# Kernel optimization log

Hardware: AMD Instinct MI355X
Metric: run time of the kernel (lower is better)

Reference implementation:

```python
import jax, jax.numpy as jnp
import numpy as np

FT_SIZE = 512
NUM_BUCKETS = 8
HID = 32
IN_FEATS = 770

def _crelu(x):
    return jnp.clip(x, 0.0, 1.0)

def setup_inputs() -> dict:
    key = jax.random.key(0)
    ks = jax.random.split(key, 8)
    B = 65536
    x = jax.random.uniform(ks[0], (B, 2 * IN_FEATS), dtype=jnp.float32)
    s = 0.05
    ft_w = jax.random.normal(ks[1], (FT_SIZE, IN_FEATS), dtype=jnp.float32) * s
    ft_b = jax.random.normal(ks[2], (FT_SIZE,), dtype=jnp.float32) * s
    h1_w = jax.random.normal(ks[3], (NUM_BUCKETS, HID, 2 * FT_SIZE), dtype=jnp.float32) * s
    h1_b = jax.random.normal(ks[4], (NUM_BUCKETS, HID), dtype=jnp.float32) * s
    h2_w = jax.random.normal(ks[5], (NUM_BUCKETS, HID, HID), dtype=jnp.float32) * s
    h2_b = jax.random.normal(ks[6], (NUM_BUCKETS, HID), dtype=jnp.float32) * s
    h3_w = jax.random.normal(ks[7], (NUM_BUCKETS, 1, HID), dtype=jnp.float32) * s
    h3_b = jnp.zeros((NUM_BUCKETS, 1), dtype=jnp.float32)
    return {"x": x, "ft_w": ft_w, "ft_b": ft_b, "h1_w": h1_w, "h1_b": h1_b,
            "h2_w": h2_w, "h2_b": h2_b, "h3_w": h3_w, "h3_b": h3_b}

def reference(x, ft_w, ft_b, h1_w, h1_b, h2_w, h2_b, h3_w, h3_b):
    stm = x[:, :IN_FEATS]          # [B, 770]
    nstm = x[:, IN_FEATS:]         # [B, 770]
    stm_ft = _crelu(stm @ ft_w.T + ft_b)    # [B, FT]
    nstm_ft = _crelu(nstm @ ft_w.T + ft_b)  # [B, FT]
    combined = jnp.concatenate([stm_ft, nstm_ft], axis=1)  # [B, 2FT]
    # bucket index from piece count (STM first 768 channels)
    pc = jnp.sum(x[:, :768], axis=1)
    bucket_idx = jnp.clip((pc * NUM_BUCKETS / 33.0).astype(jnp.int32), 0, NUM_BUCKETS - 1)  # [B]
    # compute all bucket heads (dense compute-all, matching original loop+stack)
    h = _crelu(jnp.einsum('bi,koi->bko', combined, h1_w) + h1_b)  # [B, K, 32]
    h = _crelu(jnp.einsum('bko,kpo->bkp', h, h2_w) + h2_b)        # [B, K, 32]
    all_out = jnp.einsum('bko,kpo->bkp', h, h3_w) + h3_b          # [B, K, 1]
    out = jnp.take_along_axis(all_out, bucket_idx[:, None, None], axis=1)  # [B,1,1]
    return out[:, 0, :]  # [B, 1]
```

## Files before the change

### kernel.cpp

```cpp
#include <hip/hip_runtime.h>
#include <hip/hip_bf16.h>
#include <stdint.h>


#define INF  770
#define XROW 1540
#define KP   800
#define FT   512
#define K2   1024
#define N2   256

typedef _Float16 half8 __attribute__((ext_vector_type(8)));
typedef float floatx4 __attribute__((ext_vector_type(4)));
typedef float floatx2 __attribute__((ext_vector_type(2)));

__device__ __forceinline__ float crelu_f(float v) {
    return v < 0.f ? 0.f : (v > 1.f ? 1.f : v);
}

__device__ __forceinline__ void gl_lds16(const _Float16* g, _Float16* l) {
    __builtin_amdgcn_global_load_lds(
        (__attribute__((address_space(1))) void*)(uintptr_t)(const void*)g,
        (__attribute__((address_space(3))) void*)l,
        16, 0, 0);
}

__global__ __launch_bounds__(256) void convert_w_kernel(
    const float* __restrict__ ftw, const float* __restrict__ h1w,
    _Float16* __restrict__ ftw16, _Float16* __restrict__ h1w16)
{
    int idx = blockIdx.x * 256 + threadIdx.x;
    const int FTW = FT * KP;
    if (idx < FTW) {
        int r = idx / KP, c = idx - r * KP;
        ftw16[idx] = (_Float16)(c < INF ? ftw[r * INF + c] : 0.f);
    } else {
        int j = idx - FTW;
        if (j < N2 * K2) h1w16[j] = (_Float16)h1w[j];
    }
}

__global__ __launch_bounds__(512, 4) void gemm_ft_fused(
    const float* __restrict__ x,
    const _Float16* __restrict__ Bt,
    const float* __restrict__ bias,
    _Float16* __restrict__ C,
    int* __restrict__ bucket, int B)
{
    __shared__ _Float16 lsA[128 * 32];
    __shared__ _Float16 lsB[256 * 32];
    int bid = blockIdx.x;
    int xcd = bid & 7, g = bid >> 3;
    int nt = g & 1, mt = (g >> 1) * 8 + xcd;
    int m0 = mt * 128, n0 = nt * 256;
    int tid = threadIdx.x, lane = tid & 63, w = tid >> 6;
    int rm = (w & 1) * 64, rn = (w >> 1) * 64;
    int colL = lane & 15, rowQ = lane >> 4;
    int chA = rowQ ^ ((colL >> 1) & 3);

    int arow = tid >> 2, kq = tid & 3;
    const float* asrc = (m0 < B)
        ? x + (size_t)(m0 + arow) * XROW
        : x + (size_t)(m0 - B + arow) * XROW + INF;
    _Float16* adst = lsA + arow * 32 + (kq ^ ((arow >> 1) & 3)) * 8;

    floatx4 acc[4][4] = {};
    float psum = 0.f;

    for (int kt = 0; kt < 25; ++kt) {
        int ks = kt * 32;
        half8 hv = {};
        if (kt < 24) {
            const float* p = asrc + ks + kq * 8;
            floatx2 f0 = *(const floatx2*)(p);
            floatx2 f1 = *(const floatx2*)(p + 2);
            floatx2 f2 = *(const floatx2*)(p + 4);
            floatx2 f3 = *(const floatx2*)(p + 6);
            hv[0] = (_Float16)f0.x; hv[1] = (_Float16)f0.y;
            hv[2] = (_Float16)f1.x; hv[3] = (_Float16)f1.y;
            hv[4] = (_Float16)f2.x; hv[5] = (_Float16)f2.y;
            hv[6] = (_Float16)f3.x; hv[7] = (_Float16)f3.y;
            psum += (f0.x + f0.y) + (f1.x + f1.y) + (f2.x + f2.y) + (f3.x + f3.y);
        } else if (kq == 0) {
            floatx2 f0 = *(const floatx2*)(asrc + 768);
            hv[0] = (_Float16)f0.x; hv[1] = (_Float16)f0.y;
        }
        *(half8*)adst = hv;
        #pragma unroll
        for (int p = 0; p < 2; ++p) {
            int idx = p * 512 + tid;
            int br = idx >> 2, bs = (idx & 3) ^ ((br >> 1) & 3);
            gl_lds16(Bt + (size_t)(n0 + br) * KP + ks + bs * 8, lsB + idx * 8);
        }
        asm volatile("s_waitcnt vmcnt(0)" ::: "memory");
        __syncthreads();

        half8 af[4], bf[4];
        #pragma unroll
        for (int i = 0; i < 4; ++i)
            af[i] = *(const half8*)(lsA + (rm + i * 16 + colL) * 32 + chA * 8);
        #pragma unroll
        for (int j = 0; j < 4; ++j)
            bf[j] = *(const half8*)(lsB + (rn + j * 16 + colL) * 32 + chA * 8);
        #pragma unroll
        for (int i = 0; i < 4; ++i)
            #pragma unroll
            for (int j = 0; j < 4; ++j)
                acc[i][j] = __builtin_amdgcn_mfma_f32_16x16x32_f16(af[i], bf[j], acc[i][j], 0, 0, 0);
        __syncthreads();
    }

    psum += __shfl_xor(psum, 1, 64);
    psum += __shfl_xor(psum, 2, 64);
    if (nt == 0 && m0 < B && (tid & 3) == 0) {
        int bk = (int)(psum * (8.0f / 33.0f));
        bucket[m0 + arow] = bk < 0 ? 0 : (bk > 7 ? 7 : bk);
    }

    #pragma unroll
    for (int j = 0; j < 4; ++j) {
        int gn = n0 + rn + j * 16 + colL;
        float bv = bias[gn];
        #pragma unroll
        for (int i = 0; i < 4; ++i) {
            #pragma unroll
            for (int r = 0; r < 4; ++r) {
                int gm = m0 + rm + i * 16 + rowQ * 4 + r;
                C[(size_t)gm * FT + gn] = (_Float16)crelu_f(acc[i][j][r] + bv);
            }
        }
    }
}

__global__ __launch_bounds__(512, 4) void gemm_h1_kernel(
    const _Float16* __restrict__ C1,
    const _Float16* __restrict__ Bt,
    const float* __restrict__ bias,
    float* __restrict__ H,
    int B)
{
    __shared__ _Float16 lsA[64 * 32];
    __shared__ _Float16 lsB[256 * 32];
    int m0 = blockIdx.x * 64;
    int tid = threadIdx.x, lane = tid & 63, w = tid >> 6;
    int colL = lane & 15, rowQ = lane >> 4;
    int chA = rowQ ^ ((colL >> 1) & 3);

    floatx4 acc[4][2] = {};

    for (int kt = 0; kt < 32; ++kt) {
        int ks = kt * 32;
        const _Float16* Abase = (ks < FT) ? (C1 + (size_t)m0 * FT + ks)
                                          : (C1 + (size_t)(B + m0) * FT + (ks - FT));
        if (tid < 256) {
            int br = tid >> 2, bs = (tid & 3) ^ ((br >> 1) & 3);
            gl_lds16(Abase + (size_t)br * FT + bs * 8, lsA + tid * 8);
        }
        #pragma unroll
        for (int p = 0; p < 2; ++p) {
            int idx = p * 512 + tid;
            int br = idx >> 2, bs = (idx & 3) ^ ((br >> 1) & 3);
            gl_lds16(Bt + (size_t)br * K2 + ks + bs * 8, lsB + idx * 8);
        }
        asm volatile("s_waitcnt vmcnt(0)" ::: "memory");
        __syncthreads();

        half8 af[4], bf[2];
        #pragma unroll
        for (int i = 0; i < 4; ++i)
            af[i] = *(const half8*)(lsA + (i * 16 + colL) * 32 + chA * 8);
        #pragma unroll
        for (int j = 0; j < 2; ++j)
            bf[j] = *(const half8*)(lsB + (w * 32 + j * 16 + colL) * 32 + chA * 8);
        #pragma unroll
        for (int i = 0; i < 4; ++i)
            #pragma unroll
            for (int j = 0; j < 2; ++j)
                acc[i][j] = __builtin_amdgcn_mfma_f32_16x16x32_f16(af[i], bf[j], acc[i][j], 0, 0, 0);
        __syncthreads();
    }

    #pragma unroll
    for (int j = 0; j < 2; ++j) {
        int gn = w * 32 + j * 16 + colL;
        float bv = bias[gn];
        #pragma unroll
        for (int i = 0; i < 4; ++i) {
            #pragma unroll
            for (int r = 0; r < 4; ++r) {
                int gm = m0 + i * 16 + rowQ * 4 + r;
                H[(size_t)gm * N2 + gn] = crelu_f(acc[i][j][r] + bv);
            }
        }
    }
}

__global__ __launch_bounds__(256) void tail_kernel(
    const float* __restrict__ H,
    const int* __restrict__ bucket,
    const float* __restrict__ h2w,
    const float* __restrict__ h2b,
    const float* __restrict__ h3w,
    const float* __restrict__ h3b,
    float* __restrict__ out, int B)
{
    int s = blockIdx.x * 8 + (threadIdx.x >> 5);
    int j = threadIdx.x & 31;
    if (s >= B) return;
    int k = bucket[s];
    float h1v = H[(size_t)s * N2 + k * 32 + j];
    const float* w2 = h2w + ((k * 32 + j) * 32);
    float a = h2b[k * 32 + j];
    #pragma unroll
    for (int i = 0; i < 32; ++i) a += w2[i] * __shfl(h1v, i, 32);
    a = crelu_f(a);
    float p = a * h3w[k * 32 + j];
    #pragma unroll
    for (int off = 16; off; off >>= 1) p += __shfl_down(p, off, 32);
    if (j == 0) out[s] = p + h3b[k];
}

extern "C" void kernel_launch(void* const* d_in, const int* in_sizes, int n_in,
                              void* d_out, int out_size, void* d_ws, size_t ws_size,
                              hipStream_t stream) {
    const float* x    = (const float*)d_in[0];
    const float* ftw  = (const float*)d_in[1];
    const float* ftb  = (const float*)d_in[2];
    const float* h1w  = (const float*)d_in[3];
    const float* h1b  = (const float*)d_in[4];
    const float* h2w  = (const float*)d_in[5];
    const float* h2b  = (const float*)d_in[6];
    const float* h3w  = (const float*)d_in[7];
    const float* h3b  = (const float*)d_in[8];
    float* out = (float*)d_out;

    int B = in_sizes[0] / (2 * INF);

    char* ws = (char*)d_ws;
    _Float16* C1    = (_Float16*)ws;
    size_t c1_b     = (size_t)2 * B * FT * sizeof(_Float16);
    _Float16* ftw16 = (_Float16*)(ws + c1_b);
    size_t ftw_b    = (size_t)FT * KP * sizeof(_Float16);
    _Float16* h1w16 = (_Float16*)(ws + c1_b + ftw_b);
    size_t h1w_b    = (size_t)N2 * K2 * sizeof(_Float16);
    int* bucket     = (int*)(ws + c1_b + ftw_b + h1w_b);
    size_t bk_b     = (size_t)B * sizeof(int);
    float* H        = (float*)(ws + c1_b + ftw_b + h1w_b + bk_b);

    {
        int total = FT * KP + N2 * K2;
        convert_w_kernel<<<(total + 255) / 256, 256, 0, stream>>>(ftw, h1w, ftw16, h1w16);
    }
    gemm_ft_fused<<<(2 * B / 128) * 2, 512, 0, stream>>>(x, ftw16, ftb, C1, bucket, B);
    gemm_h1_kernel<<<B / 64, 512, 0, stream>>>(C1, h1w16, h1b, H, B);
    tail_kernel<<<(B + 7) / 8, 256, 0, stream>>>(H, bucket, h2w, h2b, h3w, h3b, out, B);
}
```

Measured before the change: 800.4 us.

## Double-buffer LDS tiles in both GEMMs and raise priority during MFMA

```diff
diff --git a/kernel.cpp b/kernel.cpp
--- a/kernel.cpp
+++ b/kernel.cpp
@@ -47,8 +47,8 @@
     _Float16* __restrict__ C,
     int* __restrict__ bucket, int B)
 {
-    __shared__ _Float16 lsA[128 * 32];
-    __shared__ _Float16 lsB[256 * 32];
+    __shared__ _Float16 lsA[2][128 * 32];
+    __shared__ _Float16 lsB[2][256 * 32];
     int bid = blockIdx.x;
     int xcd = bid & 7, g = bid >> 3;
     int nt = g & 1, mt = (g >> 1) * 8 + xcd;
@@ -62,52 +62,90 @@
     const float* asrc = (m0 < B)
         ? x + (size_t)(m0 + arow) * XROW
         : x + (size_t)(m0 - B + arow) * XROW + INF;
-    _Float16* adst = lsA + arow * 32 + (kq ^ ((arow >> 1) & 3)) * 8;
+    int aoff = arow * 32 + (kq ^ ((arow >> 1) & 3)) * 8;
 
     floatx4 acc[4][4] = {};
     float psum = 0.f;
-
-    for (int kt = 0; kt < 25; ++kt) {
-        int ks = kt * 32;
-        half8 hv = {};
-        if (kt < 24) {
-            const float* p = asrc + ks + kq * 8;
-            floatx2 f0 = *(const floatx2*)(p);
-            floatx2 f1 = *(const floatx2*)(p + 2);
-            floatx2 f2 = *(const floatx2*)(p + 4);
-            floatx2 f3 = *(const floatx2*)(p + 6);
-            hv[0] = (_Float16)f0.x; hv[1] = (_Float16)f0.y;
-            hv[2] = (_Float16)f1.x; hv[3] = (_Float16)f1.y;
-            hv[4] = (_Float16)f2.x; hv[5] = (_Float16)f2.y;
-            hv[6] = (_Float16)f3.x; hv[7] = (_Float16)f3.y;
-            psum += (f0.x + f0.y) + (f1.x + f1.y) + (f2.x + f2.y) + (f3.x + f3.y);
-        } else if (kq == 0) {
-            floatx2 f0 = *(const floatx2*)(asrc + 768);
-            hv[0] = (_Float16)f0.x; hv[1] = (_Float16)f0.y;
-        }
-        *(half8*)adst = hv;
-        #pragma unroll
-        for (int p = 0; p < 2; ++p) {
-            int idx = p * 512 + tid;
-            int br = idx >> 2, bs = (idx & 3) ^ ((br >> 1) & 3);
-            gl_lds16(Bt + (size_t)(n0 + br) * KP + ks + bs * 8, lsB + idx * 8);
-        }
-        asm volatile("s_waitcnt vmcnt(0)" ::: "memory");
-        __syncthreads();
-
+    floatx2 f0, f1, f2, f3, ae = {};
+
+    {
+        const float* pp = asrc + kq * 8;
+        f0 = *(const floatx2*)(pp);
+        f1 = *(const floatx2*)(pp + 2);
+        f2 = *(const floatx2*)(pp + 4);
+        f3 = *(const floatx2*)(pp + 6);
+    }
+    #pragma unroll
+    for (int q = 0; q < 2; ++q) {
+        int idx = q * 512 + tid;
+        int br = idx >> 2, bs = (idx & 3) ^ ((br >> 1) & 3);
+        gl_lds16(Bt + (size_t)(n0 + br) * KP + bs * 8, lsB[0] + idx * 8);
+    }
+    {
+        half8 hv;
+        hv[0] = (_Float16)f0.x; hv[1] = (_Float16)f0.y;
+        hv[2] = (_Float16)f1.x; hv[3] = (_Float16)f1.y;
+        hv[4] = (_Float16)f2.x; hv[5] = (_Float16)f2.y;
+        hv[6] = (_Float16)f3.x; hv[7] = (_Float16)f3.y;
+        psum += (f0.x + f0.y) + (f1.x + f1.y) + (f2.x + f2.y) + (f3.x + f3.y);
+        *(half8*)(lsA[0] + aoff) = hv;
+    }
+    {
+        const float* pp = asrc + 32 + kq * 8;
+        f0 = *(const floatx2*)(pp);
+        f1 = *(const floatx2*)(pp + 2);
+        f2 = *(const floatx2*)(pp + 4);
+        f3 = *(const floatx2*)(pp + 6);
+    }
+    __syncthreads();
+
+    int p = 0;
+    for (int t = 0; t < 25; ++t) {
+        if (t < 24) {
+            int ks = (t + 1) * 32;
+            #pragma unroll
+            for (int q = 0; q < 2; ++q) {
+                int idx = q * 512 + tid;
+                int br = idx >> 2, bs = (idx & 3) ^ ((br >> 1) & 3);
+                gl_lds16(Bt + (size_t)(n0 + br) * KP + ks + bs * 8,
+                         lsB[p ^ 1] + idx * 8);
+            }
+            half8 hv = {};
+            if (t < 23) {
+                hv[0] = (_Float16)f0.x; hv[1] = (_Float16)f0.y;
+                hv[2] = (_Float16)f1.x; hv[3] = (_Float16)f1.y;
+                hv[4] = (_Float16)f2.x; hv[5] = (_Float16)f2.y;
+                hv[6] = (_Float16)f3.x; hv[7] = (_Float16)f3.y;
+                psum += (f0.x + f0.y) + (f1.x + f1.y) + (f2.x + f2.y) + (f3.x + f3.y);
+            } else if (kq == 0) {
+                hv[0] = (_Float16)ae.x; hv[1] = (_Float16)ae.y;
+            }
+            *(half8*)(lsA[p ^ 1] + aoff) = hv;
+            if (t < 22) {
+                const float* pp = asrc + (t + 2) * 32 + kq * 8;
+                f0 = *(const floatx2*)(pp);
+                f1 = *(const floatx2*)(pp + 2);
+                f2 = *(const floatx2*)(pp + 4);
+                f3 = *(const floatx2*)(pp + 6);
+            } else if (t == 22) {
+                if (kq == 0) ae = *(const floatx2*)(asrc + 768);
+            }
+        }
         half8 af[4], bf[4];
         #pragma unroll
         for (int i = 0; i < 4; ++i)
-            af[i] = *(const half8*)(lsA + (rm + i * 16 + colL) * 32 + chA * 8);
+            af[i] = *(const half8*)(lsA[p] + (rm + i * 16 + colL) * 32 + chA * 8);
         #pragma unroll
         for (int j = 0; j < 4; ++j)
-            bf[j] = *(const half8*)(lsB + (rn + j * 16 + colL) * 32 + chA * 8);
+            bf[j] = *(const half8*)(lsB[p] + (rn + j * 16 + colL) * 32 + chA * 8);
+        __builtin_amdgcn_s_setprio(1);
         #pragma unroll
         for (int i = 0; i < 4; ++i)
             #pragma unroll
             for (int j = 0; j < 4; ++j)
                 acc[i][j] = __builtin_amdgcn_mfma_f32_16x16x32_f16(af[i], bf[j], acc[i][j], 0, 0, 0);
-        __syncthreads();
+        __builtin_amdgcn_s_setprio(0);
+        if (t < 24) { __syncthreads(); p ^= 1; }
     }
 
     psum += __shfl_xor(psum, 1, 64);
@@ -139,8 +177,8 @@
     float* __restrict__ H,
     int B)
 {
-    __shared__ _Float16 lsA[64 * 32];
-    __shared__ _Float16 lsB[256 * 32];
+    __shared__ _Float16 lsA[2][64 * 32];
+    __shared__ _Float16 lsB[2][256 * 32];
     int m0 = blockIdx.x * 64;
     int tid = threadIdx.x, lane = tid & 63, w = tid >> 6;
     int colL = lane & 15, rowQ = lane >> 4;
@@ -148,36 +186,43 @@
 
     floatx4 acc[4][2] = {};
 
-    for (int kt = 0; kt < 32; ++kt) {
+    auto stage = [&](int kt, int b) {
         int ks = kt * 32;
         const _Float16* Abase = (ks < FT) ? (C1 + (size_t)m0 * FT + ks)
                                           : (C1 + (size_t)(B + m0) * FT + (ks - FT));
         if (tid < 256) {
             int br = tid >> 2, bs = (tid & 3) ^ ((br >> 1) & 3);
-            gl_lds16(Abase + (size_t)br * FT + bs * 8, lsA + tid * 8);
-        }
-        #pragma unroll
-        for (int p = 0; p < 2; ++p) {
-            int idx = p * 512 + tid;
+            gl_lds16(Abase + (size_t)br * FT + bs * 8, lsA[b] + tid * 8);
+        }
+        #pragma unroll
+        for (int q = 0; q < 2; ++q) {
+            int idx = q * 512 + tid;
             int br = idx >> 2, bs = (idx & 3) ^ ((br >> 1) & 3);
-            gl_lds16(Bt + (size_t)br * K2 + ks + bs * 8, lsB + idx * 8);
-        }
-        asm volatile("s_waitcnt vmcnt(0)" ::: "memory");
-        __syncthreads();
-
+            gl_lds16(Bt + (size_t)br * K2 + ks + bs * 8, lsB[b] + idx * 8);
+        }
+    };
+
+    stage(0, 0);
+    __syncthreads();
+
+    int p = 0;
+    for (int t = 0; t < 32; ++t) {
+        if (t < 31) stage(t + 1, p ^ 1);
         half8 af[4], bf[2];
         #pragma unroll
         for (int i = 0; i < 4; ++i)
-            af[i] = *(const half8*)(lsA + (i * 16 + colL) * 32 + chA * 8);
+            af[i] = *(const half8*)(lsA[p] + (i * 16 + colL) * 32 + chA * 8);
         #pragma unroll
         for (int j = 0; j < 2; ++j)
-            bf[j] = *(const half8*)(lsB + (w * 32 + j * 16 + colL) * 32 + chA * 8);
+            bf[j] = *(const half8*)(lsB[p] + (w * 32 + j * 16 + colL) * 32 + chA * 8);
+        __builtin_amdgcn_s_setprio(1);
         #pragma unroll
         for (int i = 0; i < 4; ++i)
             #pragma unroll
             for (int j = 0; j < 2; ++j)
                 acc[i][j] = __builtin_amdgcn_mfma_f32_16x16x32_f16(af[i], bf[j], acc[i][j], 0, 0, 0);
-        __syncthreads();
+        __builtin_amdgcn_s_setprio(0);
+        if (t < 31) { __syncthreads(); p ^= 1; }
     }
 
     #pragma unroll
```

Result: slower. 1.204 ms (+50.4%).

## Pre-convert x to fp16 and triple-buffer LDS in both GEMMs

Applied to the files above, without the earlier changes.

```diff
diff --git a/kernel.cpp b/kernel.cpp
--- a/kernel.cpp
+++ b/kernel.cpp
@@ -1,5 +1,4 @@
 #include <hip/hip_runtime.h>
-#include <hip/hip_bf16.h>
 #include <stdint.h>
 
 
@@ -11,8 +10,9 @@
 #define N2   256
 
 typedef _Float16 half8 __attribute__((ext_vector_type(8)));
+typedef _Float16 half4 __attribute__((ext_vector_type(4)));
+typedef _Float16 half2v __attribute__((ext_vector_type(2)));
 typedef float floatx4 __attribute__((ext_vector_type(4)));
-typedef float floatx2 __attribute__((ext_vector_type(2)));
 
 __device__ __forceinline__ float crelu_f(float v) {
     return v < 0.f ? 0.f : (v > 1.f ? 1.f : v);
@@ -24,6 +24,11 @@
         (__attribute__((address_space(3))) void*)l,
         16, 0, 0);
 }
+
+#define VMCNT(n) asm volatile("s_waitcnt vmcnt(" #n ")" ::: "memory")
+#define BAR() do { asm volatile("" ::: "memory"); \
+                   __builtin_amdgcn_s_barrier(); \
+                   asm volatile("" ::: "memory"); } while (0)
 
 __global__ __launch_bounds__(256) void convert_w_kernel(
     const float* __restrict__ ftw, const float* __restrict__ h1w,
@@ -40,15 +45,53 @@
     }
 }
 
-__global__ __launch_bounds__(512, 4) void gemm_ft_fused(
-    const float* __restrict__ x,
-    const _Float16* __restrict__ Bt,
+__global__ __launch_bounds__(256) void convert_x_kernel(
+    const float* __restrict__ x, _Float16* __restrict__ x16,
+    int* __restrict__ bucket, int B)
+{
+    int r = blockIdx.x * 4 + (threadIdx.x >> 6);
+    int l = threadIdx.x & 63;
+    const float* xr = x + (size_t)r * XROW;
+    _Float16* stm = x16 + (size_t)r * KP;
+    _Float16* nst = x16 + (size_t)(B + r) * KP;
+    float psum = 0.f;
+    for (int j = l; j < 385; j += 64) {
+        floatx4 f = *(const floatx4*)(xr + j * 4);
+        int c = j * 4;
+        if (j < 192) psum += (f.x + f.y) + (f.z + f.w);
+        if (c + 3 < INF) {
+            half4 hv = {(_Float16)f.x, (_Float16)f.y, (_Float16)f.z, (_Float16)f.w};
+            *(half4*)(stm + c) = hv;
+        } else if (c < INF) {
+            stm[768] = (_Float16)f.x; stm[769] = (_Float16)f.y;
+            nst[0]   = (_Float16)f.z; nst[1]  = (_Float16)f.w;
+        } else {
+            int cc = c - INF;
+            half2v h0 = {(_Float16)f.x, (_Float16)f.y};
+            half2v h1 = {(_Float16)f.z, (_Float16)f.w};
+            *(half2v*)(nst + cc) = h0;
+            *(half2v*)(nst + cc + 2) = h1;
+        }
+    }
+    half2v z = {};
+    if (l < 15)                *(half2v*)(stm + INF + 2 * l) = z;
+    else if (l >= 16 && l < 31) *(half2v*)(nst + INF + 2 * (l - 16)) = z;
+    #pragma unroll
+    for (int off = 1; off < 64; off <<= 1) psum += __shfl_xor(psum, off, 64);
+    if (l == 0) {
+        int bk = (int)(psum * (8.0f / 33.0f));
+        bucket[r] = bk < 0 ? 0 : (bk > 7 ? 7 : bk);
+    }
+}
+
+__global__ __launch_bounds__(512, 4) void gemm_ft_p(
+    const _Float16* __restrict__ A,
+    const _Float16* __restrict__ Bw,
     const float* __restrict__ bias,
-    _Float16* __restrict__ C,
-    int* __restrict__ bucket, int B)
-{
-    __shared__ _Float16 lsA[128 * 32];
-    __shared__ _Float16 lsB[256 * 32];
+    _Float16* __restrict__ C)
+{
+    __shared__ _Float16 lsA[3][128 * 32];
+    __shared__ _Float16 lsB[3][256 * 32];
     int bid = blockIdx.x;
     int xcd = bid & 7, g = bid >> 3;
     int nt = g & 1, mt = (g >> 1) * 8 + xcd;
@@ -58,64 +101,58 @@
     int colL = lane & 15, rowQ = lane >> 4;
     int chA = rowQ ^ ((colL >> 1) & 3);
 
-    int arow = tid >> 2, kq = tid & 3;
-    const float* asrc = (m0 < B)
-        ? x + (size_t)(m0 + arow) * XROW
-        : x + (size_t)(m0 - B + arow) * XROW + INF;
-    _Float16* adst = lsA + arow * 32 + (kq ^ ((arow >> 1) & 3)) * 8;
+    int ar = tid >> 2, as_ = (tid & 3) ^ ((ar >> 1) & 3);
+    const _Float16* pa = A + (size_t)(m0 + ar) * KP + as_ * 8;
+    const _Float16* pb = Bw + (size_t)(n0 + ar) * KP + as_ * 8;
 
     floatx4 acc[4][4] = {};
-    float psum = 0.f;
-
-    for (int kt = 0; kt < 25; ++kt) {
-        int ks = kt * 32;
-        half8 hv = {};
-        if (kt < 24) {
-            const float* p = asrc + ks + kq * 8;
-            floatx2 f0 = *(const floatx2*)(p);
-            floatx2 f1 = *(const floatx2*)(p + 2);
-            floatx2 f2 = *(const floatx2*)(p + 4);
-            floatx2 f3 = *(const floatx2*)(p + 6);
-            hv[0] = (_Float16)f0.x; hv[1] = (_Float16)f0.y;
-            hv[2] = (_Float16)f1.x; hv[3] = (_Float16)f1.y;
-            hv[4] = (_Float16)f2.x; hv[5] = (_Float16)f2.y;
-            hv[6] = (_Float16)f3.x; hv[7] = (_Float16)f3.y;
-            psum += (f0.x + f0.y) + (f1.x + f1.y) + (f2.x + f2.y) + (f3.x + f3.y);
-        } else if (kq == 0) {
-            floatx2 f0 = *(const floatx2*)(asrc + 768);
-            hv[0] = (_Float16)f0.x; hv[1] = (_Float16)f0.y;
-        }
-        *(half8*)adst = hv;
-        #pragma unroll
-        for (int p = 0; p < 2; ++p) {
-            int idx = p * 512 + tid;
-            int br = idx >> 2, bs = (idx & 3) ^ ((br >> 1) & 3);
-            gl_lds16(Bt + (size_t)(n0 + br) * KP + ks + bs * 8, lsB + idx * 8);
-        }
-        asm volatile("s_waitcnt vmcnt(0)" ::: "memory");
-        __syncthreads();
-
+
+    auto STAGE = [&](int kt, _Float16* dA, _Float16* dB) {
+        gl_lds16(pa + kt * 32, dA + tid * 8);
+        gl_lds16(pb + kt * 32, dB + tid * 8);
+        gl_lds16(pb + 128 * KP + kt * 32, dB + (512 + tid) * 8);
+    };
+    auto COMPUTE = [&](const _Float16* bA, const _Float16* bB) {
         half8 af[4], bf[4];
         #pragma unroll
         for (int i = 0; i < 4; ++i)
-            af[i] = *(const half8*)(lsA + (rm + i * 16 + colL) * 32 + chA * 8);
+            af[i] = *(const half8*)(bA + (rm + i * 16 + colL) * 32 + chA * 8);
         #pragma unroll
         for (int j = 0; j < 4; ++j)
-            bf[j] = *(const half8*)(lsB + (rn + j * 16 + colL) * 32 + chA * 8);
+            bf[j] = *(const half8*)(bB + (rn + j * 16 + colL) * 32 + chA * 8);
+        __builtin_amdgcn_s_setprio(1);
         #pragma unroll
         for (int i = 0; i < 4; ++i)
             #pragma unroll
             for (int j = 0; j < 4; ++j)
                 acc[i][j] = __builtin_amdgcn_mfma_f32_16x16x32_f16(af[i], bf[j], acc[i][j], 0, 0, 0);
-        __syncthreads();
-    }
-
-    psum += __shfl_xor(psum, 1, 64);
-    psum += __shfl_xor(psum, 2, 64);
-    if (nt == 0 && m0 < B && (tid & 3) == 0) {
-        int bk = (int)(psum * (8.0f / 33.0f));
-        bucket[m0 + arow] = bk < 0 ? 0 : (bk > 7 ? 7 : bk);
-    }
+        __builtin_amdgcn_s_setprio(0);
+    };
+
+    _Float16 *cA0 = lsA[0], *cA1 = lsA[1], *cA2 = lsA[2];
+    _Float16 *cB0 = lsB[0], *cB1 = lsB[1], *cB2 = lsB[2];
+
+    STAGE(0, cA0, cB0);
+    STAGE(1, cA1, cB1);
+
+    for (int t = 0; t < 23; ++t) {
+        STAGE(t + 2, cA2, cB2);
+        VMCNT(6);
+        BAR();
+        COMPUTE(cA0, cB0);
+        BAR();
+        _Float16* tA = cA0; cA0 = cA1; cA1 = cA2; cA2 = tA;
+        _Float16* tB = cB0; cB0 = cB1; cB1 = cB2; cB2 = tB;
+    }
+    VMCNT(3);
+    BAR();
+    COMPUTE(cA0, cB0);
+    BAR();
+    { _Float16* tA = cA0; cA0 = cA1; cA1 = cA2; cA2 = tA;
+      _Float16* tB = cB0; cB0 = cB1; cB1 = cB2; cB2 = tB; }
+    VMCNT(0);
+    BAR();
+    COMPUTE(cA0, cB0);
 
     #pragma unroll
     for (int j = 0; j < 4; ++j) {
@@ -132,63 +169,85 @@
     }
 }
 
-__global__ __launch_bounds__(512, 4) void gemm_h1_kernel(
+__global__ __launch_bounds__(512, 4) void gemm_h1_p(
     const _Float16* __restrict__ C1,
-    const _Float16* __restrict__ Bt,
+    const _Float16* __restrict__ Bw,
     const float* __restrict__ bias,
     float* __restrict__ H,
     int B)
 {
-    __shared__ _Float16 lsA[64 * 32];
-    __shared__ _Float16 lsB[256 * 32];
-    int m0 = blockIdx.x * 64;
+    __shared__ _Float16 lsA[3][128 * 32];
+    __shared__ _Float16 lsB[3][256 * 32];
+    int m0 = blockIdx.x * 128;
     int tid = threadIdx.x, lane = tid & 63, w = tid >> 6;
+    int rm = (w & 1) * 64, rn = (w >> 1) * 64;
     int colL = lane & 15, rowQ = lane >> 4;
     int chA = rowQ ^ ((colL >> 1) & 3);
 
-    floatx4 acc[4][2] = {};
-
-    for (int kt = 0; kt < 32; ++kt) {
-        int ks = kt * 32;
-        const _Float16* Abase = (ks < FT) ? (C1 + (size_t)m0 * FT + ks)
-                                          : (C1 + (size_t)(B + m0) * FT + (ks - FT));
-        if (tid < 256) {
-            int br = tid >> 2, bs = (tid & 3) ^ ((br >> 1) & 3);
-            gl_lds16(Abase + (size_t)br * FT + bs * 8, lsA + tid * 8);
-        }
-        #pragma unroll
-        for (int p = 0; p < 2; ++p) {
-            int idx = p * 512 + tid;
-            int br = idx >> 2, bs = (idx & 3) ^ ((br >> 1) & 3);
-            gl_lds16(Bt + (size_t)br * K2 + ks + bs * 8, lsB + idx * 8);
-        }
-        asm volatile("s_waitcnt vmcnt(0)" ::: "memory");
-        __syncthreads();
-
-        half8 af[4], bf[2];
+    int ar = tid >> 2, as_ = (tid & 3) ^ ((ar >> 1) & 3);
+    const _Float16* pa  = C1 + (size_t)(m0 + ar) * FT + as_ * 8;
+    const _Float16* paH = C1 + (size_t)(B + m0 + ar) * FT + as_ * 8;
+    const _Float16* pb  = Bw + (size_t)ar * K2 + as_ * 8;
+
+    floatx4 acc[4][4] = {};
+
+    auto STAGE = [&](int kt, _Float16* dA, _Float16* dB) {
+        const _Float16* a = (kt < 16) ? (pa + kt * 32) : (paH + (kt - 16) * 32);
+        gl_lds16(a, dA + tid * 8);
+        gl_lds16(pb + kt * 32, dB + tid * 8);
+        gl_lds16(pb + 128 * K2 + kt * 32, dB + (512 + tid) * 8);
+    };
+    auto COMPUTE = [&](const _Float16* bA, const _Float16* bB) {
+        half8 af[4], bf[4];
         #pragma unroll
         for (int i = 0; i < 4; ++i)
-            af[i] = *(const half8*)(lsA + (i * 16 + colL) * 32 + chA * 8);
-        #pragma unroll
-        for (int j = 0; j < 2; ++j)
-            bf[j] = *(const half8*)(lsB + (w * 32 + j * 16 + colL) * 32 + chA * 8);
+            af[i] = *(const half8*)(bA + (rm + i * 16 + colL) * 32 + chA * 8);
+        #pragma unroll
+        for (int j = 0; j < 4; ++j)
+            bf[j] = *(const half8*)(bB + (rn + j * 16 + colL) * 32 + chA * 8);
+        __builtin_amdgcn_s_setprio(1);
         #pragma unroll
         for (int i = 0; i < 4; ++i)
             #pragma unroll
-            for (int j = 0; j < 2; ++j)
+            for (int j = 0; j < 4; ++j)
                 acc[i][j] = __builtin_amdgcn_mfma_f32_16x16x32_f16(af[i], bf[j], acc[i][j], 0, 0, 0);
-        __syncthreads();
-    }
-
-    #pragma unroll
-    for (int j = 0; j < 2; ++j) {
-        int gn = w * 32 + j * 16 + colL;
+        __builtin_amdgcn_s_setprio(0);
+    };
+
+    _Float16 *cA0 = lsA[0], *cA1 = lsA[1], *cA2 = lsA[2];
+    _Float16 *cB0 = lsB[0], *cB1 = lsB[1], *cB2 = lsB[2];
+
+    STAGE(0, cA0, cB0);
+    STAGE(1, cA1, cB1);
+
+    for (int t = 0; t < 30; ++t) {
+        STAGE(t + 2, cA2, cB2);
+        VMCNT(6);
+        BAR();
+        COMPUTE(cA0, cB0);
+        BAR();
+        _Float16* tA = cA0; cA0 = cA1; cA1 = cA2; cA2 = tA;
+        _Float16* tB = cB0; cB0 = cB1; cB1 = cB2; cB2 = tB;
+    }
+    VMCNT(3);
+    BAR();
+    COMPUTE(cA0, cB0);
+    BAR();
+    { _Float16* tA = cA0; cA0 = cA1; cA1 = cA2; cA2 = tA;
+      _Float16* tB = cB0; cB0 = cB1; cB1 = cB2; cB2 = tB; }
+    VMCNT(0);
+    BAR();
+    COMPUTE(cA0, cB0);
+
+    #pragma unroll
+    for (int j = 0; j < 4; ++j) {
+        int gn = rn + j * 16 + colL;
         float bv = bias[gn];
         #pragma unroll
         for (int i = 0; i < 4; ++i) {
             #pragma unroll
             for (int r = 0; r < 4; ++r) {
-                int gm = m0 + i * 16 + rowQ * 4 + r;
+                int gm = m0 + rm + i * 16 + rowQ * 4 + r;
                 H[(size_t)gm * N2 + gn] = crelu_f(acc[i][j][r] + bv);
             }
         }
@@ -246,12 +305,15 @@
     int* bucket     = (int*)(ws + c1_b + ftw_b + h1w_b);
     size_t bk_b     = (size_t)B * sizeof(int);
     float* H        = (float*)(ws + c1_b + ftw_b + h1w_b + bk_b);
+    size_t H_b      = (size_t)B * N2 * sizeof(float);
+    _Float16* x16   = (_Float16*)(ws + c1_b + ftw_b + h1w_b + bk_b + H_b);
 
     {
         int total = FT * KP + N2 * K2;
         convert_w_kernel<<<(total + 255) / 256, 256, 0, stream>>>(ftw, h1w, ftw16, h1w16);
     }
-    gemm_ft_fused<<<(2 * B / 128) * 2, 512, 0, stream>>>(x, ftw16, ftb, C1, bucket, B);
-    gemm_h1_kernel<<<B / 64, 512, 0, stream>>>(C1, h1w16, h1b, H, B);
+    convert_x_kernel<<<B / 4, 256, 0, stream>>>(x, x16, bucket, B);
+    gemm_ft_p<<<(2 * B / 128) * 2, 512, 0, stream>>>(x16, ftw16, ftb, C1);
+    gemm_h1_p<<<B / 128, 512, 0, stream>>>(C1, h1w16, h1b, H, B);
     tail_kernel<<<(B + 7) / 8, 256, 0, stream>>>(H, bucket, h2w, h2b, h3w, h3b, out, B);
 }
```

After: 834.5 us. 1.04x slower.
